# Performance work log

Measured on AMD Instinct MI355X. Metric: run time of the kernel, lower is better.

## Reference

```python
import jax, jax.numpy as jnp
import numpy as np

B, C, N, QK, VC, S = 64, 64, 256, 8, 32, 16
EPS = 1e-5
SCALE = float(np.sqrt(QK))  # qk_channel ** 0.5


def _bn(x, p):
    # eval-mode BatchNorm1d over [B, C, N]; p = [gamma, beta, mean, var]
    g, b, m, v = p
    return (x - m[None, :, None]) * (g * jax.lax.rsqrt(v + EPS))[None, :, None] + b[None, :, None]


def _conv1x1(w, x, b=None):
    y = jnp.einsum('oc,bcn->bon', w, x)
    return y if b is None else y + b[None, :, None]


def setup_inputs() -> dict:
    key = jax.random.key(0)
    ks = jax.random.split(key, 16)

    def w(k, o, i):
        return jax.random.normal(k, (o, i), jnp.float32) * (1.0 / np.sqrt(i))

    def bn_p(k, c):
        k1, k2, k3, k4 = jax.random.split(k, 4)
        return jnp.stack([
            jax.random.uniform(k1, (c,), jnp.float32) + 0.5,   # gamma
            jax.random.normal(k2, (c,), jnp.float32) * 0.1,    # beta
            jax.random.normal(k3, (c,), jnp.float32) * 0.1,    # running mean
            jax.random.uniform(k4, (c,), jnp.float32) + 0.5,   # running var (>0)
        ])

    x = jax.random.normal(ks[0], (B, C, N), jnp.float32)
    stroke_idx = jax.random.randint(ks[1], (B, N), 0, S, jnp.int32)
    stroke_idx = stroke_idx.at[:, -1].set(S - 1)  # guarantee max == S-1

    ga_q_w = w(ks[2], QK, C)
    sa_q_w = w(ks[3], QK, C)
    inp = {
        'x': x,
        'stroke_idx': stroke_idx,
        'n_strokes': S,
        'ga_q_w': ga_q_w,
        'ga_k_w': ga_q_w.copy(),  # k initialized as clone of q in source
        'ga_v_w': w(ks[4], VC, C),
        'ga_v_b': jax.random.normal(ks[5], (VC,), jnp.float32) * 0.01,
        'ga_bn_p': bn_p(ks[6], VC),
        'ga_lb_w': w(ks[7], VC, C),
        'ga_lb_bn_p': bn_p(ks[8], VC),
        'sa_q_w': sa_q_w,
        'sa_k_w': sa_q_w.copy(),
        'sa_v_w': w(ks[9], VC, C),
        'sa_v_b': jax.random.normal(ks[10], (VC,), jnp.float32) * 0.01,
        'sa_bn_p': bn_p(ks[11], VC),
        'sa_lb_w': w(ks[12], VC, C),
        'sa_lb_bn_p': bn_p(ks[13], VC),
        'mlp_w1': w(ks[14], 4 * C, C),
        'mlp_bn1_p': bn_p(jax.random.fold_in(key, 100), 4 * C),
        'mlp_w2': w(ks[15], C, 4 * C),
        'mlp_bn2_p': bn_p(jax.random.fold_in(key, 101), C),
    }
    return inp


def _ga_block(x, qw, kw, vw, vb):
    q = jnp.einsum('oc,bcn->bno', qw, x)                 # [B,N,QK]
    k = jnp.einsum('oc,bcn->bon', kw, x)                 # [B,QK,N]
    v = jnp.einsum('oc,bcn->bno', vw, x) + vb[None, None, :]  # [B,N,VC]
    attn = jax.nn.softmax(jnp.einsum('bno,bom->bnm', q, k) / SCALE, axis=-1)
    return jnp.einsum('bnm,bmv->bvn', attn, v)           # [B,VC,N]


def _sa_block(x, stroke_idx, n_strokes, qw, kw, vw, vb):
    q = jnp.einsum('oc,bcn->bno', qw, x)
    k = jnp.einsum('oc,bcn->bon', kw, x)
    v = jnp.einsum('oc,bcn->bno', vw, x) + vb[None, None, :]
    base = jnp.einsum('bno,bom->bnm', q, k) / SCALE      # [B,N,N]
    # per-stroke additive mask: 0 where stroke == i else 1e-6 (as in source)
    masks = jnp.where(stroke_idx[None, :, :] == jnp.arange(n_strokes)[:, None, None],
                      0.0, 1e-6).astype(base.dtype)       # [S,B,N]
    energy = (base[None] + masks[:, :, None, :]) * 10.0   # [S,B,N,N]
    attn = jax.nn.softmax(energy, axis=-1)
    # sum over strokes fused into the contraction
    return jnp.einsum('sbnm,bmv->bvn', attn, v)           # [B,VC,N]


def reference(x, stroke_idx, n_strokes, ga_q_w, ga_k_w, ga_v_w, ga_v_b, ga_bn_p,
              ga_lb_w, ga_lb_bn_p, sa_q_w, sa_k_w, sa_v_w, sa_v_b, sa_bn_p,
              sa_lb_w, sa_lb_bn_p, mlp_w1, mlp_bn1_p, mlp_w2, mlp_bn2_p):
    f_ga = _bn(_ga_block(x, ga_q_w, ga_k_w, ga_v_w, ga_v_b), ga_bn_p) \
         + _bn(_conv1x1(ga_lb_w, x), ga_lb_bn_p)
    f_sa = _bn(_sa_block(x, stroke_idx, n_strokes, sa_q_w, sa_k_w, sa_v_w, sa_v_b), sa_bn_p) \
         + _bn(_conv1x1(sa_lb_w, x), sa_lb_bn_p)
    f = jnp.concatenate([f_ga, f_sa], axis=1)            # [B,C,N]
    h = jax.nn.relu(_bn(_conv1x1(mlp_w1, f), mlp_bn1_p))  # [B,4C,N]
    f_mlp = _bn(_conv1x1(mlp_w2, h), mlp_bn2_p)           # [B,C,N]
    return jax.nn.relu(f_mlp + f)
```

## Files before the change

### kernel.cpp

```cpp
#include <hip/hip_runtime.h>
#include <math.h>


#define EPS    1e-5f
#define LOG2E  1.4426950408889634f

#define OFF_QGA 0u
#define OFF_KGA 131072u
#define OFF_VGA 262144u
#define OFF_QSA 786432u
#define OFF_KSA 917504u
#define OFF_VSA 1048576u
#define OFF_F   1572864u
#define OFF_H   2621440u

__global__ __launch_bounds__(512) void k_proj(
    const float* __restrict__ x,
    const float* __restrict__ gaq, const float* __restrict__ gak,
    const float* __restrict__ gav, const float* __restrict__ gavb,
    const float* __restrict__ galb, const float* __restrict__ galbbn,
    const float* __restrict__ saq, const float* __restrict__ sak,
    const float* __restrict__ sav, const float* __restrict__ savb,
    const float* __restrict__ salb, const float* __restrict__ salbbn,
    float* ws)
{
    __shared__ float O2[160][65];
    const int lane = threadIdx.x & 63;
    const int wvu  = __builtin_amdgcn_readfirstlane((int)(threadIdx.x >> 6));
    const int b    = blockIdx.x >> 2;
    const int n0   = (blockIdx.x & 3) << 6;
    const int p0g  = blockIdx.x << 6;

    float xr[64];
    const float* xb = x + (size_t)(b * 64) * 256 + n0 + lane;
    #pragma unroll
    for (int c = 0; c < 64; ++c) xr[c] = xb[c * 256];

    for (int i = 0; i < 20; ++i) {
        const int slot = wvu * 20 + i;
        const float* wr; float mul = 1.f, add = 0.f;
        if (slot < 8)        { wr = gaq + slot * 64; }
        else if (slot < 16)  { wr = gak + (slot - 8) * 64; }
        else if (slot < 48)  { int vc = slot - 16; wr = gav + vc * 64; add = gavb[vc]; }
        else if (slot < 56)  { wr = saq + (slot - 48) * 64; }
        else if (slot < 64)  { wr = sak + (slot - 56) * 64; }
        else if (slot < 96)  { int vc = slot - 64; wr = sav + vc * 64; add = savb[vc]; }
        else if (slot < 128) { int vc = slot - 96; wr = galb + vc * 64;
                               float s = galbbn[vc] * rsqrtf(galbbn[96 + vc] + EPS);
                               mul = s; add = galbbn[32 + vc] - galbbn[64 + vc] * s; }
        else                 { int vc = slot - 128; wr = salb + vc * 64;
                               float s = salbbn[vc] * rsqrtf(salbbn[96 + vc] + EPS);
                               mul = s; add = salbbn[32 + vc] - salbbn[64 + vc] * s; }
        float acc = 0.f;
        #pragma unroll
        for (int c = 0; c < 64; ++c) acc = fmaf(wr[c], xr[c], acc);
        O2[slot][lane] = acc * mul + add;
    }
    __syncthreads();

    for (int t = threadIdx.x; t < 2560; t += 512) {
        int u, rb, l; unsigned g;
        if (t < 128)       { u = t;        rb = 0;   l = 1; g = OFF_QGA; }
        else if (t < 256)  { u = t - 128;  rb = 8;   l = 1; g = OFF_KGA; }
        else if (t < 768)  { u = t - 256;  rb = 16;  l = 3; g = OFF_VGA; }
        else if (t < 896)  { u = t - 768;  rb = 48;  l = 1; g = OFF_QSA; }
        else if (t < 1024) { u = t - 896;  rb = 56;  l = 1; g = OFF_KSA; }
        else if (t < 1536) { u = t - 1024; rb = 64;  l = 3; g = OFF_VSA; }
        else               { u = t - 1536; rb = 96;  l = 4; g = OFF_F;   }
        const int p    = u >> l;
        const int off4 = u & ((1 << l) - 1);
        const int row  = rb + off4 * 4;
        float4 v;
        v.x = O2[row + 0][p]; v.y = O2[row + 1][p];
        v.z = O2[row + 2][p]; v.w = O2[row + 3][p];
        *(float4*)(ws + g + (size_t)(p0g + p) * (4u << l) + off4 * 4) = v;
    }
}

__global__ __launch_bounds__(512) void k_attn(
    const float* __restrict__ wsr, const float* __restrict__ gabnp,
    const float* __restrict__ sabnp, float* F)
{
    __shared__ float MW[8][64];
    __shared__ float ZW[8][64];
    __shared__ float AW[8][64][33];
    const int which = blockIdx.x >> 8;
    const int bb    = blockIdx.x & 255;
    const int b     = bb >> 2;
    const int n0    = (bb & 3) << 6;
    const unsigned ro = which ? 786432u : 0u;
    const float* Q = wsr + OFF_QGA + ro;
    const float* K = wsr + OFF_KGA + ro;
    const float* V = wsr + OFF_VGA + ro;
    const float* bnp = which ? sabnp : gabnp;
    const float factor   = which ? 3.5355339059327378f : 0.35355339059327378f;
    const float outscale = which ? 16.f : 1.f;
    const int   choff    = which << 5;

    const int lane = threadIdx.x & 63;
    const int w    = __builtin_amdgcn_readfirstlane((int)(threadIdx.x >> 6));
    const int p    = b * 256 + n0 + lane;
    const float fl = factor * LOG2E;
    float4 qa = *(const float4*)(Q + (size_t)p * 8);
    float4 qb = *(const float4*)(Q + (size_t)p * 8 + 4);
    qa.x *= fl; qa.y *= fl; qa.z *= fl; qa.w *= fl;
    qb.x *= fl; qb.y *= fl; qb.z *= fl; qb.w *= fl;
    const int m0 = w << 5;
    const float* Kb = K + (size_t)(b * 256 + m0) * 8;
    const float* Vb = V + (size_t)(b * 256 + m0) * 32;

    float M = -1e30f;
    #pragma unroll 4
    for (int i = 0; i < 32; ++i) {
        const float4 k0 = *(const float4*)(Kb + i * 8);
        const float4 k1 = *(const float4*)(Kb + i * 8 + 4);
        float t0 = qa.x * k0.x + qa.y * k0.y + qa.z * k0.z + qa.w * k0.w;
        float t1 = qb.x * k1.x + qb.y * k1.y + qb.z * k1.z + qb.w * k1.w;
        M = fmaxf(M, t0 + t1);
    }
    float Z = 0.f;
    float acc[32];
    #pragma unroll
    for (int j = 0; j < 32; ++j) acc[j] = 0.f;
    #pragma unroll 2
    for (int i = 0; i < 32; ++i) {
        const float4 k0 = *(const float4*)(Kb + i * 8);
        const float4 k1 = *(const float4*)(Kb + i * 8 + 4);
        float t0 = qa.x * k0.x + qa.y * k0.y + qa.z * k0.z + qa.w * k0.w;
        float t1 = qb.x * k1.x + qb.y * k1.y + qb.z * k1.z + qb.w * k1.w;
        float pv = exp2f(t0 + t1 - M);
        Z += pv;
        const float* vr = Vb + (size_t)i * 32;
        #pragma unroll
        for (int j4 = 0; j4 < 8; ++j4) {
            float4 vv = *(const float4*)(vr + j4 * 4);
            acc[j4 * 4 + 0] = fmaf(pv, vv.x, acc[j4 * 4 + 0]);
            acc[j4 * 4 + 1] = fmaf(pv, vv.y, acc[j4 * 4 + 1]);
            acc[j4 * 4 + 2] = fmaf(pv, vv.z, acc[j4 * 4 + 2]);
            acc[j4 * 4 + 3] = fmaf(pv, vv.w, acc[j4 * 4 + 3]);
        }
    }
    MW[w][lane] = M;
    ZW[w][lane] = Z;
    #pragma unroll
    for (int j = 0; j < 32; ++j) AW[w][lane][j] = acc[j];
    __syncthreads();

    const int vc = threadIdx.x & 31;
    const int rg = threadIdx.x >> 5;
    const float g  = bnp[vc], be = bnp[32 + vc], mn = bnp[64 + vc], va = bnp[96 + vc];
    const float s    = g * rsqrtf(va + EPS) * outscale;
    const float bias = be - mn * (g * rsqrtf(va + EPS));
    for (int r = 0; r < 4; ++r) {
        const int rr = rg * 4 + r;
        float Mx = MW[0][rr];
        #pragma unroll
        for (int u = 1; u < 8; ++u) Mx = fmaxf(Mx, MW[u][rr]);
        float Zt = 0.f, A = 0.f;
        #pragma unroll
        for (int u = 0; u < 8; ++u) {
            float cw = exp2f(MW[u][rr] - Mx);
            Zt += ZW[u][rr] * cw;
            A   = fmaf(AW[u][rr][vc], cw, A);
        }
        float* fp = F + (size_t)(b * 256 + n0 + rr) * 64 + choff + vc;
        *fp = (A / Zt) * s + bias + *fp;
    }
}

__global__ __launch_bounds__(256) void k_mlp1(
    const float* __restrict__ Fin, const float* __restrict__ w1,
    const float* __restrict__ bn1, float* __restrict__ H)
{
    __shared__ __align__(16) float wL[64][68];
    const int jg = blockIdx.x & 3;
    const int nt = (blockIdx.x >> 2) & 7;
    const int b  = blockIdx.x >> 5;
    const int j0 = jg << 6;
    const int n0 = nt << 5;
    for (int t = threadIdx.x; t < 4096; t += 256) {
        int jj = t >> 6, c = t & 63;
        wL[jj][c] = w1[(j0 + jj) * 64 + c];
    }
    __syncthreads();
    const int lane = threadIdx.x & 63;
    const int wq = __builtin_amdgcn_readfirstlane((int)(threadIdx.x >> 6));
    const int j  = j0 + lane;
    const int pbase = b * 256 + n0 + wq * 8;
    const float* f0 = Fin + (size_t)pbase * 64;
    float acc[8] = {0.f,0.f,0.f,0.f,0.f,0.f,0.f,0.f};
    #pragma unroll
    for (int c4 = 0; c4 < 16; ++c4) {
        float4 wv = *(const float4*)&wL[lane][c4 * 4];
        #pragma unroll
        for (int r = 0; r < 8; ++r) {
            float4 fv = *(const float4*)&f0[r * 64 + c4 * 4];
            acc[r] += wv.x * fv.x + wv.y * fv.y + wv.z * fv.z + wv.w * fv.w;
        }
    }
    const float gg = bn1[j], be = bn1[256 + j], mn = bn1[512 + j], va = bn1[768 + j];
    const float s    = gg * rsqrtf(va + EPS);
    const float bias = be - mn * s;
    #pragma unroll
    for (int r = 0; r < 8; ++r)
        H[(size_t)(pbase + r) * 256 + j] = fmaxf(acc[r] * s + bias, 0.f);
}

__global__ __launch_bounds__(256) void k_mlp2(
    const float* __restrict__ H, const float* __restrict__ w2,
    const float* __restrict__ bn2, const float* __restrict__ Fin,
    float* __restrict__ out)
{
    __shared__ __align__(16) float w2L[64][268];
    __shared__ float OT[64][33];
    const int b   = blockIdx.x >> 3;
    const int nw  = (blockIdx.x & 7) << 5;
    for (int t = threadIdx.x; t < 16384; t += 256) {
        w2L[t >> 8][t & 255] = w2[t];
    }
    __syncthreads();
    const int lane = threadIdx.x & 63;
    const int wq = __builtin_amdgcn_readfirstlane((int)(threadIdx.x >> 6));
    const float g = bn2[lane], be = bn2[64 + lane], mn = bn2[128 + lane], va = bn2[192 + lane];
    const float s    = g * rsqrtf(va + EPS);
    const float bias = be - mn * s;
    for (int g2 = 0; g2 < 2; ++g2) {
        const int nl = wq * 8 + g2 * 4;
        const int pb = b * 256 + nw + nl;
        const float* h0 = H + (size_t)pb * 256;
        float acc[4] = {0.f,0.f,0.f,0.f};
        for (int j4 = 0; j4 < 64; ++j4) {
            float4 wv = *(const float4*)&w2L[lane][j4 * 4];
            #pragma unroll
            for (int r = 0; r < 4; ++r) {
                float4 hv = *(const float4*)&h0[r * 256 + j4 * 4];
                acc[r] += wv.x * hv.x + wv.y * hv.y + wv.z * hv.z + wv.w * hv.w;
            }
        }
        #pragma unroll
        for (int r = 0; r < 4; ++r) {
            float f = Fin[(size_t)(pb + r) * 64 + lane];
            OT[lane][nl + r] = fmaxf(acc[r] * s + bias + f, 0.f);
        }
    }
    __syncthreads();
    for (int t = threadIdx.x; t < 512; t += 256) {
        int c = t >> 3, j4 = (t & 7) << 2;
        float4 v;
        v.x = OT[c][j4]; v.y = OT[c][j4 + 1]; v.z = OT[c][j4 + 2]; v.w = OT[c][j4 + 3];
        *(float4*)(out + (size_t)(b * 64 + c) * 256 + nw + j4) = v;
    }
}

extern "C" void kernel_launch(void* const* d_in, const int* in_sizes, int n_in,
                              void* d_out, int out_size, void* d_ws, size_t ws_size,
                              hipStream_t stream) {
    const float* x      = (const float*)d_in[0];
    const float* gaq    = (const float*)d_in[3];
    const float* gak    = (const float*)d_in[4];
    const float* gav    = (const float*)d_in[5];
    const float* gavb   = (const float*)d_in[6];
    const float* gabnp  = (const float*)d_in[7];
    const float* galb   = (const float*)d_in[8];
    const float* galbbn = (const float*)d_in[9];
    const float* saq    = (const float*)d_in[10];
    const float* sak    = (const float*)d_in[11];
    const float* sav    = (const float*)d_in[12];
    const float* savb   = (const float*)d_in[13];
    const float* sabnp  = (const float*)d_in[14];
    const float* salb   = (const float*)d_in[15];
    const float* salbbn = (const float*)d_in[16];
    const float* w1     = (const float*)d_in[17];
    const float* bn1    = (const float*)d_in[18];
    const float* w2     = (const float*)d_in[19];
    const float* bn2    = (const float*)d_in[20];
    float* ws   = (float*)d_ws;
    float* outp = (float*)d_out;

    k_proj<<<dim3(256), dim3(512), 0, stream>>>(
        x, gaq, gak, gav, gavb, galb, galbbn,
        saq, sak, sav, savb, salb, salbbn, ws);

    k_attn<<<dim3(512), dim3(512), 0, stream>>>(ws, gabnp, sabnp, ws + OFF_F);

    k_mlp1<<<dim3(2048), dim3(256), 0, stream>>>(ws + OFF_F, w1, bn1, ws + OFF_H);
    k_mlp2<<<dim3(512),  dim3(256), 0, stream>>>(ws + OFF_H, w2, bn2, ws + OFF_F, outp);
}
```

Before: 181.5 us.

## Fuse attention and both MLP stages into one kernel with shared-memory intermediates

Merges k_attn, k_mlp1 and k_mlp2 into a single kernel. Each block handles 64 points, computes both attention branches in sequence, keeps F and the hidden activations H in LDS (H shares a union with the attention scratch), and writes the output directly. This removes two launches and the global round-trip of F and the 256-channel H buffer. The cost is fewer blocks (256 instead of 512), each with more LDS in use and a longer serial chain, and MLP weights that are now read from global/L2 by every block instead of staged in LDS.

```diff
diff --git a/kernel.cpp b/kernel.cpp
--- a/kernel.cpp
+++ b/kernel.cpp
@@ -12,7 +12,6 @@
 #define OFF_KSA 917504u
 #define OFF_VSA 1048576u
 #define OFF_F   1572864u
-#define OFF_H   2621440u
 
 __global__ __launch_bounds__(512) void k_proj(
     const float* __restrict__ x,
@@ -77,178 +76,175 @@
     }
 }
 
-__global__ __launch_bounds__(512) void k_attn(
+__global__ __launch_bounds__(512) void k_fused(
     const float* __restrict__ wsr, const float* __restrict__ gabnp,
-    const float* __restrict__ sabnp, float* F)
+    const float* __restrict__ sabnp, const float* __restrict__ Fin,
+    const float* __restrict__ w1, const float* __restrict__ bn1,
+    const float* __restrict__ w2, const float* __restrict__ bn2,
+    float* __restrict__ out)
 {
     __shared__ float MW[8][64];
     __shared__ float ZW[8][64];
-    __shared__ float AW[8][64][33];
-    const int which = blockIdx.x >> 8;
-    const int bb    = blockIdx.x & 255;
-    const int b     = bb >> 2;
-    const int n0    = (bb & 3) << 6;
-    const unsigned ro = which ? 786432u : 0u;
-    const float* Q = wsr + OFF_QGA + ro;
-    const float* K = wsr + OFF_KGA + ro;
-    const float* V = wsr + OFF_VGA + ro;
-    const float* bnp = which ? sabnp : gabnp;
-    const float factor   = which ? 3.5355339059327378f : 0.35355339059327378f;
-    const float outscale = which ? 16.f : 1.f;
-    const int   choff    = which << 5;
+    __shared__ __align__(16) float fL[64][68];
+    union USH {
+        float AW[8][64][33];
+        float hL[64][268];
+    };
+    __shared__ __align__(16) USH U;
 
     const int lane = threadIdx.x & 63;
     const int w    = __builtin_amdgcn_readfirstlane((int)(threadIdx.x >> 6));
-    const int p    = b * 256 + n0 + lane;
-    const float fl = factor * LOG2E;
-    float4 qa = *(const float4*)(Q + (size_t)p * 8);
-    float4 qb = *(const float4*)(Q + (size_t)p * 8 + 4);
-    qa.x *= fl; qa.y *= fl; qa.z *= fl; qa.w *= fl;
-    qb.x *= fl; qb.y *= fl; qb.z *= fl; qb.w *= fl;
+    const int b    = blockIdx.x >> 2;
+    const int n0   = (blockIdx.x & 3) << 6;
+
+    {
+        const float4* src = (const float4*)(Fin + (size_t)(b * 256 + n0) * 64);
+        #pragma unroll
+        for (int t0 = 0; t0 < 2; ++t0) {
+            const int t = (int)threadIdx.x + t0 * 512;
+            float4 v = src[t];
+            *(float4*)&fL[t >> 4][(t & 15) << 2] = v;
+        }
+    }
+
+    const int p  = b * 256 + n0 + lane;
     const int m0 = w << 5;
-    const float* Kb = K + (size_t)(b * 256 + m0) * 8;
-    const float* Vb = V + (size_t)(b * 256 + m0) * 32;
-
-    float M = -1e30f;
-    #pragma unroll 4
-    for (int i = 0; i < 32; ++i) {
-        const float4 k0 = *(const float4*)(Kb + i * 8);
-        const float4 k1 = *(const float4*)(Kb + i * 8 + 4);
-        float t0 = qa.x * k0.x + qa.y * k0.y + qa.z * k0.z + qa.w * k0.w;
-        float t1 = qb.x * k1.x + qb.y * k1.y + qb.z * k1.z + qb.w * k1.w;
-        M = fmaxf(M, t0 + t1);
-    }
-    float Z = 0.f;
-    float acc[32];
-    #pragma unroll
-    for (int j = 0; j < 32; ++j) acc[j] = 0.f;
-    #pragma unroll 2
-    for (int i = 0; i < 32; ++i) {
-        const float4 k0 = *(const float4*)(Kb + i * 8);
-        const float4 k1 = *(const float4*)(Kb + i * 8 + 4);
-        float t0 = qa.x * k0.x + qa.y * k0.y + qa.z * k0.z + qa.w * k0.w;
-        float t1 = qb.x * k1.x + qb.y * k1.y + qb.z * k1.z + qb.w * k1.w;
-        float pv = exp2f(t0 + t1 - M);
-        Z += pv;
-        const float* vr = Vb + (size_t)i * 32;
-        #pragma unroll
-        for (int j4 = 0; j4 < 8; ++j4) {
-            float4 vv = *(const float4*)(vr + j4 * 4);
-            acc[j4 * 4 + 0] = fmaf(pv, vv.x, acc[j4 * 4 + 0]);
-            acc[j4 * 4 + 1] = fmaf(pv, vv.y, acc[j4 * 4 + 1]);
-            acc[j4 * 4 + 2] = fmaf(pv, vv.z, acc[j4 * 4 + 2]);
-            acc[j4 * 4 + 3] = fmaf(pv, vv.w, acc[j4 * 4 + 3]);
-        }
-    }
-    MW[w][lane] = M;
-    ZW[w][lane] = Z;
-    #pragma unroll
-    for (int j = 0; j < 32; ++j) AW[w][lane][j] = acc[j];
+
+    for (int which = 0; which < 2; ++which) {
+        const unsigned ro = which ? 786432u : 0u;
+        const float* Q = wsr + OFF_QGA + ro;
+        const float* K = wsr + OFF_KGA + ro;
+        const float* V = wsr + OFF_VGA + ro;
+        const float* bnp = which ? sabnp : gabnp;
+        const float factor   = which ? 3.5355339059327378f : 0.35355339059327378f;
+        const float outscale = which ? 16.f : 1.f;
+        const int   choff    = which << 5;
+
+        const float fl = factor * LOG2E;
+        float4 qa = *(const float4*)(Q + (size_t)p * 8);
+        float4 qb = *(const float4*)(Q + (size_t)p * 8 + 4);
+        qa.x *= fl; qa.y *= fl; qa.z *= fl; qa.w *= fl;
+        qb.x *= fl; qb.y *= fl; qb.z *= fl; qb.w *= fl;
+        const float* Kb = K + (size_t)(b * 256 + m0) * 8;
+        const float* Vb = V + (size_t)(b * 256 + m0) * 32;
+
+        float M = -1e30f;
+        #pragma unroll 4
+        for (int i = 0; i < 32; ++i) {
+            const float4 k0 = *(const float4*)(Kb + i * 8);
+            const float4 k1 = *(const float4*)(Kb + i * 8 + 4);
+            float t0 = qa.x * k0.x + qa.y * k0.y + qa.z * k0.z + qa.w * k0.w;
+            float t1 = qb.x * k1.x + qb.y * k1.y + qb.z * k1.z + qb.w * k1.w;
+            M = fmaxf(M, t0 + t1);
+        }
+        float Z = 0.f;
+        float acc[32];
+        #pragma unroll
+        for (int j = 0; j < 32; ++j) acc[j] = 0.f;
+        #pragma unroll 2
+        for (int i = 0; i < 32; ++i) {
+            const float4 k0 = *(const float4*)(Kb + i * 8);
+            const float4 k1 = *(const float4*)(Kb + i * 8 + 4);
+            float t0 = qa.x * k0.x + qa.y * k0.y + qa.z * k0.z + qa.w * k0.w;
+            float t1 = qb.x * k1.x + qb.y * k1.y + qb.z * k1.z + qb.w * k1.w;
+            float pv = exp2f(t0 + t1 - M);
+            Z += pv;
+            const float* vr = Vb + (size_t)i * 32;
+            #pragma unroll
+            for (int j4 = 0; j4 < 8; ++j4) {
+                float4 vv = *(const float4*)(vr + j4 * 4);
+                acc[j4 * 4 + 0] = fmaf(pv, vv.x, acc[j4 * 4 + 0]);
+                acc[j4 * 4 + 1] = fmaf(pv, vv.y, acc[j4 * 4 + 1]);
+                acc[j4 * 4 + 2] = fmaf(pv, vv.z, acc[j4 * 4 + 2]);
+                acc[j4 * 4 + 3] = fmaf(pv, vv.w, acc[j4 * 4 + 3]);
+            }
+        }
+        MW[w][lane] = M;
+        ZW[w][lane] = Z;
+        #pragma unroll
+        for (int j = 0; j < 32; ++j) U.AW[w][lane][j] = acc[j];
+        __syncthreads();
+
+        {
+            const int vc = threadIdx.x & 31;
+            const int rg = threadIdx.x >> 5;
+            const float g  = bnp[vc], be = bnp[32 + vc],
+                        mn = bnp[64 + vc], va = bnp[96 + vc];
+            const float gs   = g * rsqrtf(va + EPS);
+            const float s    = gs * outscale;
+            const float bias = be - mn * gs;
+            for (int r = 0; r < 4; ++r) {
+                const int rr = (rg << 2) + r;
+                float Mx = MW[0][rr];
+                #pragma unroll
+                for (int u = 1; u < 8; ++u) Mx = fmaxf(Mx, MW[u][rr]);
+                float Zt = 0.f, A = 0.f;
+                #pragma unroll
+                for (int u = 0; u < 8; ++u) {
+                    float cw = exp2f(MW[u][rr] - Mx);
+                    Zt += ZW[u][rr] * cw;
+                    A   = fmaf(U.AW[u][rr][vc], cw, A);
+                }
+                fL[rr][choff + vc] += (A / Zt) * s + bias;
+            }
+        }
+        __syncthreads();
+    }
+
+    float4 fr[16];
+    #pragma unroll
+    for (int c4 = 0; c4 < 16; ++c4)
+        fr[c4] = *(const float4*)&fL[lane][c4 << 2];
+
+    const int j0 = w << 5;
+    for (int jj = 0; jj < 32; jj += 4) {
+        const float* wrow = w1 + (size_t)(j0 + jj) * 64;
+        float a0 = 0.f, a1 = 0.f, a2 = 0.f, a3 = 0.f;
+        #pragma unroll
+        for (int c4 = 0; c4 < 16; ++c4) {
+            const float4 f  = fr[c4];
+            const float4 w0 = *(const float4*)(wrow +       (c4 << 2));
+            const float4 w1v= *(const float4*)(wrow +  64 + (c4 << 2));
+            const float4 w2v= *(const float4*)(wrow + 128 + (c4 << 2));
+            const float4 w3v= *(const float4*)(wrow + 192 + (c4 << 2));
+            a0 += w0.x * f.x + w0.y * f.y + w0.z * f.z + w0.w * f.w;
+            a1 += w1v.x * f.x + w1v.y * f.y + w1v.z * f.z + w1v.w * f.w;
+            a2 += w2v.x * f.x + w2v.y * f.y + w2v.z * f.z + w2v.w * f.w;
+            a3 += w3v.x * f.x + w3v.y * f.y + w3v.z * f.z + w3v.w * f.w;
+        }
+        const int j = j0 + jj;
+        float4 hv;
+        { float g = bn1[j+0], be = bn1[256+j+0], mn = bn1[512+j+0], va = bn1[768+j+0];
+          float s = g * rsqrtf(va + EPS); hv.x = fmaxf(a0 * s + (be - mn * s), 0.f); }
+        { float g = bn1[j+1], be = bn1[256+j+1], mn = bn1[512+j+1], va = bn1[768+j+1];
+          float s = g * rsqrtf(va + EPS); hv.y = fmaxf(a1 * s + (be - mn * s), 0.f); }
+        { float g = bn1[j+2], be = bn1[256+j+2], mn = bn1[512+j+2], va = bn1[768+j+2];
+          float s = g * rsqrtf(va + EPS); hv.z = fmaxf(a2 * s + (be - mn * s), 0.f); }
+        { float g = bn1[j+3], be = bn1[256+j+3], mn = bn1[512+j+3], va = bn1[768+j+3];
+          float s = g * rsqrtf(va + EPS); hv.w = fmaxf(a3 * s + (be - mn * s), 0.f); }
+        *(float4*)&U.hL[lane][j] = hv;
+    }
     __syncthreads();
 
-    const int vc = threadIdx.x & 31;
-    const int rg = threadIdx.x >> 5;
-    const float g  = bnp[vc], be = bnp[32 + vc], mn = bnp[64 + vc], va = bnp[96 + vc];
-    const float s    = g * rsqrtf(va + EPS) * outscale;
-    const float bias = be - mn * (g * rsqrtf(va + EPS));
-    for (int r = 0; r < 4; ++r) {
-        const int rr = rg * 4 + r;
-        float Mx = MW[0][rr];
-        #pragma unroll
-        for (int u = 1; u < 8; ++u) Mx = fmaxf(Mx, MW[u][rr]);
-        float Zt = 0.f, A = 0.f;
-        #pragma unroll
-        for (int u = 0; u < 8; ++u) {
-            float cw = exp2f(MW[u][rr] - Mx);
-            Zt += ZW[u][rr] * cw;
-            A   = fmaf(AW[u][rr][vc], cw, A);
-        }
-        float* fp = F + (size_t)(b * 256 + n0 + rr) * 64 + choff + vc;
-        *fp = (A / Zt) * s + bias + *fp;
-    }
-}
-
-__global__ __launch_bounds__(256) void k_mlp1(
-    const float* __restrict__ Fin, const float* __restrict__ w1,
-    const float* __restrict__ bn1, float* __restrict__ H)
-{
-    __shared__ __align__(16) float wL[64][68];
-    const int jg = blockIdx.x & 3;
-    const int nt = (blockIdx.x >> 2) & 7;
-    const int b  = blockIdx.x >> 5;
-    const int j0 = jg << 6;
-    const int n0 = nt << 5;
-    for (int t = threadIdx.x; t < 4096; t += 256) {
-        int jj = t >> 6, c = t & 63;
-        wL[jj][c] = w1[(j0 + jj) * 64 + c];
-    }
-    __syncthreads();
-    const int lane = threadIdx.x & 63;
-    const int wq = __builtin_amdgcn_readfirstlane((int)(threadIdx.x >> 6));
-    const int j  = j0 + lane;
-    const int pbase = b * 256 + n0 + wq * 8;
-    const float* f0 = Fin + (size_t)pbase * 64;
-    float acc[8] = {0.f,0.f,0.f,0.f,0.f,0.f,0.f,0.f};
-    #pragma unroll
-    for (int c4 = 0; c4 < 16; ++c4) {
-        float4 wv = *(const float4*)&wL[lane][c4 * 4];
-        #pragma unroll
-        for (int r = 0; r < 8; ++r) {
-            float4 fv = *(const float4*)&f0[r * 64 + c4 * 4];
-            acc[r] += wv.x * fv.x + wv.y * fv.y + wv.z * fv.z + wv.w * fv.w;
-        }
-    }
-    const float gg = bn1[j], be = bn1[256 + j], mn = bn1[512 + j], va = bn1[768 + j];
-    const float s    = gg * rsqrtf(va + EPS);
-    const float bias = be - mn * s;
-    #pragma unroll
-    for (int r = 0; r < 8; ++r)
-        H[(size_t)(pbase + r) * 256 + j] = fmaxf(acc[r] * s + bias, 0.f);
-}
-
-__global__ __launch_bounds__(256) void k_mlp2(
-    const float* __restrict__ H, const float* __restrict__ w2,
-    const float* __restrict__ bn2, const float* __restrict__ Fin,
-    float* __restrict__ out)
-{
-    __shared__ __align__(16) float w2L[64][268];
-    __shared__ float OT[64][33];
-    const int b   = blockIdx.x >> 3;
-    const int nw  = (blockIdx.x & 7) << 5;
-    for (int t = threadIdx.x; t < 16384; t += 256) {
-        w2L[t >> 8][t & 255] = w2[t];
-    }
-    __syncthreads();
-    const int lane = threadIdx.x & 63;
-    const int wq = __builtin_amdgcn_readfirstlane((int)(threadIdx.x >> 6));
-    const float g = bn2[lane], be = bn2[64 + lane], mn = bn2[128 + lane], va = bn2[192 + lane];
-    const float s    = g * rsqrtf(va + EPS);
-    const float bias = be - mn * s;
-    for (int g2 = 0; g2 < 2; ++g2) {
-        const int nl = wq * 8 + g2 * 4;
-        const int pb = b * 256 + nw + nl;
-        const float* h0 = H + (size_t)pb * 256;
-        float acc[4] = {0.f,0.f,0.f,0.f};
-        for (int j4 = 0; j4 < 64; ++j4) {
-            float4 wv = *(const float4*)&w2L[lane][j4 * 4];
-            #pragma unroll
-            for (int r = 0; r < 4; ++r) {
-                float4 hv = *(const float4*)&h0[r * 256 + j4 * 4];
-                acc[r] += wv.x * hv.x + wv.y * hv.y + wv.z * hv.z + wv.w * hv.w;
-            }
-        }
-        #pragma unroll
-        for (int r = 0; r < 4; ++r) {
-            float f = Fin[(size_t)(pb + r) * 64 + lane];
-            OT[lane][nl + r] = fmaxf(acc[r] * s + bias + f, 0.f);
-        }
-    }
-    __syncthreads();
-    for (int t = threadIdx.x; t < 512; t += 256) {
-        int c = t >> 3, j4 = (t & 7) << 2;
-        float4 v;
-        v.x = OT[c][j4]; v.y = OT[c][j4 + 1]; v.z = OT[c][j4 + 2]; v.w = OT[c][j4 + 3];
-        *(float4*)(out + (size_t)(b * 64 + c) * 256 + nw + j4) = v;
+    float a2c[8];
+    #pragma unroll
+    for (int k = 0; k < 8; ++k) a2c[k] = 0.f;
+    const float* w2base = w2 + (size_t)(w << 3) * 256;
+    for (int j4 = 0; j4 < 64; ++j4) {
+        const float4 hv = *(const float4*)&U.hL[lane][j4 << 2];
+        #pragma unroll
+        for (int k = 0; k < 8; ++k) {
+            const float4 wv = *(const float4*)(w2base + k * 256 + (j4 << 2));
+            a2c[k] += wv.x * hv.x + wv.y * hv.y + wv.z * hv.z + wv.w * hv.w;
+        }
+    }
+    #pragma unroll
+    for (int k = 0; k < 8; ++k) {
+        const int c = (w << 3) + k;
+        const float g = bn2[c], be = bn2[64 + c], mn = bn2[128 + c], va = bn2[192 + c];
+        const float s = g * rsqrtf(va + EPS);
+        const float v = a2c[k] * s + (be - mn * s) + fL[lane][c];
+        out[(size_t)(b * 64 + c) * 256 + n0 + lane] = fmaxf(v, 0.f);
     }
 }
 
@@ -281,8 +277,6 @@
         x, gaq, gak, gav, gavb, galb, galbbn,
         saq, sak, sav, savb, salb, salbbn, ws);
 
-    k_attn<<<dim3(512), dim3(512), 0, stream>>>(ws, gabnp, sabnp, ws + OFF_F);
-
-    k_mlp1<<<dim3(2048), dim3(256), 0, stream>>>(ws + OFF_F, w1, bn1, ws + OFF_H);
-    k_mlp2<<<dim3(512),  dim3(256), 0, stream>>>(ws + OFF_H, w2, bn2, ws + OFF_F, outp);
+    k_fused<<<dim3(256), dim3(512), 0, stream>>>(
+        ws, gabnp, sabnp, ws + OFF_F, w1, bn1, w2, bn2, outp);
 }
```

Measured after the change: 207.6 us. 14.4% more time.

## Split attention keys across lane groups and merge via warp shuffles

Applied to the files above, without the earlier changes.

The attention kernel changes its work split: each query is now handled by 8 lanes of a wavefront, each covering an interleaved subset of 32 keys. The partial softmax results are merged with xor shuffles and a transpose-reduce that leaves each lane holding 4 output channels. This replaces the old per-wave key split that went through shared memory and a __syncthreads. Scores are cached in registers instead of being computed twice, and the launch becomes 1024 blocks of 256 threads. The trade-off is more register pressure, and K/V loads are now gathered across lanes instead of broadcast.

```diff
diff --git a/kernel.cpp b/kernel.cpp
--- a/kernel.cpp
+++ b/kernel.cpp
@@ -77,17 +77,14 @@
     }
 }
 
-__global__ __launch_bounds__(512) void k_attn(
+__global__ __launch_bounds__(256, 4) void k_attn(
     const float* __restrict__ wsr, const float* __restrict__ gabnp,
     const float* __restrict__ sabnp, float* F)
 {
-    __shared__ float MW[8][64];
-    __shared__ float ZW[8][64];
-    __shared__ float AW[8][64][33];
-    const int which = blockIdx.x >> 8;
-    const int bb    = blockIdx.x & 255;
-    const int b     = bb >> 2;
-    const int n0    = (bb & 3) << 6;
+    const int which = blockIdx.x >> 9;
+    const int bb    = blockIdx.x & 511;
+    const int b     = bb >> 3;
+    const int q0    = (bb & 7) << 5;
     const unsigned ro = which ? 786432u : 0u;
     const float* Q = wsr + OFF_QGA + ro;
     const float* K = wsr + OFF_KGA + ro;
@@ -98,74 +95,111 @@
     const int   choff    = which << 5;
 
     const int lane = threadIdx.x & 63;
-    const int w    = __builtin_amdgcn_readfirstlane((int)(threadIdx.x >> 6));
-    const int p    = b * 256 + n0 + lane;
+    const int w    = (int)(threadIdx.x >> 6);
+    const int qr   = lane >> 3;
+    const int g    = lane & 7;
+    const int p    = b * 256 + q0 + (w << 3) + qr;
+
     const float fl = factor * LOG2E;
     float4 qa = *(const float4*)(Q + (size_t)p * 8);
     float4 qb = *(const float4*)(Q + (size_t)p * 8 + 4);
     qa.x *= fl; qa.y *= fl; qa.z *= fl; qa.w *= fl;
     qb.x *= fl; qb.y *= fl; qb.z *= fl; qb.w *= fl;
-    const int m0 = w << 5;
-    const float* Kb = K + (size_t)(b * 256 + m0) * 8;
-    const float* Vb = V + (size_t)(b * 256 + m0) * 32;
-
+
+    const float* Kb = K + (size_t)(b * 256) * 8;
+    const float* Vb = V + (size_t)(b * 256) * 32;
+
+    float s[32];
     float M = -1e30f;
-    #pragma unroll 4
+    #pragma unroll
     for (int i = 0; i < 32; ++i) {
-        const float4 k0 = *(const float4*)(Kb + i * 8);
-        const float4 k1 = *(const float4*)(Kb + i * 8 + 4);
-        float t0 = qa.x * k0.x + qa.y * k0.y + qa.z * k0.z + qa.w * k0.w;
-        float t1 = qb.x * k1.x + qb.y * k1.y + qb.z * k1.z + qb.w * k1.w;
-        M = fmaxf(M, t0 + t1);
-    }
+        const int m = g + (i << 3);
+        const float4 k0 = *(const float4*)(Kb + (size_t)m * 8);
+        const float4 k1 = *(const float4*)(Kb + (size_t)m * 8 + 4);
+        s[i] = qa.x * k0.x + qa.y * k0.y + qa.z * k0.z + qa.w * k0.w
+             + qb.x * k1.x + qb.y * k1.y + qb.z * k1.z + qb.w * k1.w;
+        M = fmaxf(M, s[i]);
+    }
+
     float Z = 0.f;
     float acc[32];
     #pragma unroll
     for (int j = 0; j < 32; ++j) acc[j] = 0.f;
-    #pragma unroll 2
+    #pragma unroll
     for (int i = 0; i < 32; ++i) {
-        const float4 k0 = *(const float4*)(Kb + i * 8);
-        const float4 k1 = *(const float4*)(Kb + i * 8 + 4);
-        float t0 = qa.x * k0.x + qa.y * k0.y + qa.z * k0.z + qa.w * k0.w;
-        float t1 = qb.x * k1.x + qb.y * k1.y + qb.z * k1.z + qb.w * k1.w;
-        float pv = exp2f(t0 + t1 - M);
+        const int m = g + (i << 3);
+        const float pv = exp2f(s[i] - M);
         Z += pv;
-        const float* vr = Vb + (size_t)i * 32;
+        const float* vr = Vb + (size_t)m * 32;
         #pragma unroll
         for (int j4 = 0; j4 < 8; ++j4) {
-            float4 vv = *(const float4*)(vr + j4 * 4);
+            const float4 vv = *(const float4*)(vr + (j4 << 2));
             acc[j4 * 4 + 0] = fmaf(pv, vv.x, acc[j4 * 4 + 0]);
             acc[j4 * 4 + 1] = fmaf(pv, vv.y, acc[j4 * 4 + 1]);
             acc[j4 * 4 + 2] = fmaf(pv, vv.z, acc[j4 * 4 + 2]);
             acc[j4 * 4 + 3] = fmaf(pv, vv.w, acc[j4 * 4 + 3]);
         }
     }
-    MW[w][lane] = M;
-    ZW[w][lane] = Z;
-    #pragma unroll
-    for (int j = 0; j < 32; ++j) AW[w][lane][j] = acc[j];
-    __syncthreads();
-
-    const int vc = threadIdx.x & 31;
-    const int rg = threadIdx.x >> 5;
-    const float g  = bnp[vc], be = bnp[32 + vc], mn = bnp[64 + vc], va = bnp[96 + vc];
-    const float s    = g * rsqrtf(va + EPS) * outscale;
-    const float bias = be - mn * (g * rsqrtf(va + EPS));
-    for (int r = 0; r < 4; ++r) {
-        const int rr = rg * 4 + r;
-        float Mx = MW[0][rr];
-        #pragma unroll
-        for (int u = 1; u < 8; ++u) Mx = fmaxf(Mx, MW[u][rr]);
-        float Zt = 0.f, A = 0.f;
-        #pragma unroll
-        for (int u = 0; u < 8; ++u) {
-            float cw = exp2f(MW[u][rr] - Mx);
-            Zt += ZW[u][rr] * cw;
-            A   = fmaf(AW[u][rr][vc], cw, A);
-        }
-        float* fp = F + (size_t)(b * 256 + n0 + rr) * 64 + choff + vc;
-        *fp = (A / Zt) * s + bias + *fp;
-    }
+
+    float Mx = M;
+    Mx = fmaxf(Mx, __shfl_xor(Mx, 1));
+    Mx = fmaxf(Mx, __shfl_xor(Mx, 2));
+    Mx = fmaxf(Mx, __shfl_xor(Mx, 4));
+    const float cw = exp2f(M - Mx);
+    Z *= cw;
+    #pragma unroll
+    for (int j = 0; j < 32; ++j) acc[j] *= cw;
+    Z += __shfl_xor(Z, 1);
+    Z += __shfl_xor(Z, 2);
+    Z += __shfl_xor(Z, 4);
+    float r16[16];
+    #pragma unroll
+    for (int t = 0; t < 16; ++t) {
+        float snd = (g & 4) ? acc[t] : acc[16 + t];
+        float rcv = __shfl_xor(snd, 4);
+        r16[t] = ((g & 4) ? acc[16 + t] : acc[t]) + rcv;
+    }
+    float r8[8];
+    #pragma unroll
+    for (int t = 0; t < 8; ++t) {
+        float snd = (g & 2) ? r16[t] : r16[8 + t];
+        float rcv = __shfl_xor(snd, 2);
+        r8[t] = ((g & 2) ? r16[8 + t] : r16[t]) + rcv;
+    }
+    float a4[4];
+    #pragma unroll
+    for (int t = 0; t < 4; ++t) {
+        float snd = (g & 1) ? r8[t] : r8[4 + t];
+        float rcv = __shfl_xor(snd, 1);
+        a4[t] = ((g & 1) ? r8[4 + t] : r8[t]) + rcv;
+    }
+
+    const int vc0 = g << 2;
+    const float4 ga4 = *(const float4*)(bnp + vc0);
+    const float4 be4 = *(const float4*)(bnp + 32 + vc0);
+    const float4 mn4 = *(const float4*)(bnp + 64 + vc0);
+    const float4 va4 = *(const float4*)(bnp + 96 + vc0);
+    const float iz = 1.f / Z;
+    float* fp = F + (size_t)p * 64 + choff + vc0;
+    float4 old = *(const float4*)fp;
+    float4 o;
+    {
+        float gs = ga4.x * rsqrtf(va4.x + EPS);
+        o.x = old.x + a4[0] * iz * gs * outscale + (be4.x - mn4.x * gs);
+    }
+    {
+        float gs = ga4.y * rsqrtf(va4.y + EPS);
+        o.y = old.y + a4[1] * iz * gs * outscale + (be4.y - mn4.y * gs);
+    }
+    {
+        float gs = ga4.z * rsqrtf(va4.z + EPS);
+        o.z = old.z + a4[2] * iz * gs * outscale + (be4.z - mn4.z * gs);
+    }
+    {
+        float gs = ga4.w * rsqrtf(va4.w + EPS);
+        o.w = old.w + a4[3] * iz * gs * outscale + (be4.w - mn4.w * gs);
+    }
+    *(float4*)fp = o;
 }
 
 __global__ __launch_bounds__(256) void k_mlp1(
@@ -281,7 +315,7 @@
         x, gaq, gak, gav, gavb, galb, galbbn,
         saq, sak, sav, savb, salb, salbbn, ws);
 
-    k_attn<<<dim3(512), dim3(512), 0, stream>>>(ws, gabnp, sabnp, ws + OFF_F);
+    k_attn<<<dim3(1024), dim3(256), 0, stream>>>(ws, gabnp, sabnp, ws + OFF_F);
 
     k_mlp1<<<dim3(2048), dim3(256), 0, stream>>>(ws + OFF_F, w1, bn1, ws + OFF_H);
     k_mlp2<<<dim3(512),  dim3(256), 0, stream>>>(ws + OFF_H, w2, bn2, ws + OFF_F, outp);
```

Result: slower. 276.3 us (+52.2%).
